# Optimization experiments

Measured on AMD Instinct MI355X. Metric: run time of the kernel, lower is better.

## Reference

```python
import jax, jax.numpy as jnp
import numpy as np

H = 4096          # hidden_size
NIN = 17          # RFSIZE*RFSIZE + ADDINPUT + NBACTIONS = 9+4+4
NA = 4            # NBACTIONS


def setup_inputs() -> dict:
    key = jax.random.key(0)
    ks = jax.random.split(key, 12)
    return {
        "x": jax.random.normal(ks[0], (1, NIN), jnp.float32),
        "hidden": 0.1 * jax.random.normal(ks[1], (1, H), jnp.float32),
        "hebb": 0.01 * jax.random.normal(ks[2], (H, H), jnp.float32),
        "i2h_w": 0.1 * jax.random.normal(ks[3], (H, NIN), jnp.float32),
        "i2h_b": 0.1 * jax.random.normal(ks[4], (H,), jnp.float32),
        "w": 0.01 * jax.random.uniform(ks[5], (H, H), jnp.float32),
        "alpha": 0.01 * jax.random.uniform(ks[6], (H, H), jnp.float32),
        "eta": 0.01 * jnp.ones((1,), jnp.float32),
        "h2o_w": 0.1 * jax.random.normal(ks[7], (NA, H), jnp.float32),
        "h2o_b": 0.1 * jax.random.normal(ks[8], (NA,), jnp.float32),
        "h2v_w": 0.1 * jax.random.normal(ks[9], (1, H), jnp.float32),
        "h2v_b": 0.1 * jax.random.normal(ks[10], (1,), jnp.float32),
    }


def reference(x, hidden, hebb, i2h_w, i2h_b, w, alpha, eta, h2o_w, h2o_b, h2v_w, h2v_b):
    # plastic RNN step: h = tanh(i2h(x) + hidden @ (w + alpha*hebb))
    h = jnp.tanh(x @ i2h_w.T + i2h_b + hidden @ (w + alpha * hebb))  # [1,H]
    # Hebbian trace update: (1-eta)*hebb + eta * outer(hidden, h)
    hebb_new = (1.0 - eta) * hebb + eta * (hidden[0][:, None] * h[0][None, :])  # [H,H]
    activout = jax.nn.softmax(h @ h2o_w.T + h2o_b, axis=-1)  # [1,NA]
    valueout = h @ h2v_w.T + h2v_b                           # [1,1]
    return activout, valueout, h, hebb_new
```

## Files before the change

### kernel.cpp

```cpp
#include <hip/hip_runtime.h>

#define HDIM 4096
#define NIN 17
#define NA 4

constexpr int TB = 256;
constexpr int CPT = 4;
constexpr int BXC = HDIM / (TB * CPT);
constexpr int NCHUNK = 256;
constexpr int RPC = HDIM / NCHUNK;
constexpr size_t NELEM = (size_t)HDIM * HDIM;

__global__ __launch_bounds__(TB, 4)
void k_matvec(const float* __restrict__ w, const float* __restrict__ alpha,
              const float* __restrict__ hebb, const float* __restrict__ hidden,
              float* __restrict__ partial, float* __restrict__ acc5) {
    if (blockIdx.x == 0 && blockIdx.y == 0 && threadIdx.x < 8) acc5[threadIdx.x] = 0.f;

    const int col0 = (blockIdx.x * TB + threadIdx.x) * CPT;
    const int row0 = blockIdx.y * RPC;
    const size_t base = (size_t)row0 * HDIM + col0;
    const float* __restrict__ wp = w + base;
    const float* __restrict__ ap = alpha + base;
    const float* __restrict__ bp = hebb + base;
    float4 acc = make_float4(0.f, 0.f, 0.f, 0.f);
#pragma unroll 8
    for (int r = 0; r < RPC; ++r) {
        const float hv = hidden[row0 + r];
        const size_t off = (size_t)r * HDIM;
        const float4 wv = *(const float4*)(wp + off);
        const float4 av = *(const float4*)(ap + off);
        const float4 bv = *(const float4*)(bp + off);
        acc.x += hv * (wv.x + av.x * bv.x);
        acc.y += hv * (wv.y + av.y * bv.y);
        acc.z += hv * (wv.z + av.z * bv.z);
        acc.w += hv * (wv.w + av.w * bv.w);
    }
    *(float4*)(partial + (size_t)blockIdx.y * HDIM + col0) = acc;
}

__global__ __launch_bounds__(256)
void k_hact(const float* __restrict__ partial, const float* __restrict__ x,
            const float* __restrict__ i2h_w, const float* __restrict__ i2h_b,
            const float* __restrict__ h2o_w, const float* __restrict__ h2v_w,
            float* __restrict__ h_f, float* __restrict__ h_out,
            float* __restrict__ acc5) {
    const int tid = threadIdx.x;
    const int j = blockIdx.x * 256 + tid;
    float s = 0.f;
#pragma unroll 16
    for (int c = 0; c < NCHUNK; ++c) s += partial[(size_t)c * HDIM + j];
    float z = i2h_b[j] + s;
#pragma unroll
    for (int k = 0; k < NIN; ++k) z += x[k] * i2h_w[j * NIN + k];
    const float h = tanhf(z);
    h_f[j] = h;
    h_out[j] = h;

    float d[NA + 1];
#pragma unroll
    for (int a = 0; a < NA; ++a) d[a] = h * h2o_w[(size_t)a * HDIM + j];
    d[NA] = h * h2v_w[j];

    __shared__ float red[256];
#pragma unroll
    for (int a = 0; a < NA + 1; ++a) {
        red[tid] = d[a];
        __syncthreads();
        for (int sft = 128; sft > 0; sft >>= 1) {
            if (tid < sft) red[tid] += red[tid + sft];
            __syncthreads();
        }
        if (tid == 0) atomicAdd(acc5 + a, red[0]);
        __syncthreads();
    }
}

__global__ __launch_bounds__(256)
void k_hebb(const float* __restrict__ hebb, const float* __restrict__ hidden,
            const float* __restrict__ h_f, const float* __restrict__ eta,
            float* __restrict__ hebb_out) {
    const size_t t = (size_t)blockIdx.x * 256 + threadIdx.x;
    const size_t s = 4 * t + 3;
    const float e = eta[0];
    const float om = 1.f - e;

    if (t == 0) {
        const float hv0 = e * hidden[0];
        hebb_out[0] = om * hebb[0] + hv0 * h_f[0];
        hebb_out[1] = om * hebb[1] + hv0 * h_f[1];
        hebb_out[2] = om * hebb[2] + hv0 * h_f[2];
    }

    if (s + 3 < NELEM) {
        const float b0 = hebb[s];
        const float4 bv = *(const float4*)(hebb + s + 1);
        const float b[4] = {b0, bv.x, bv.y, bv.z};
        float v[4];
#pragma unroll
        for (int k = 0; k < 4; ++k) {
            const size_t m = s + (size_t)k;
            const int i = (int)(m >> 12);
            const int jj = (int)(m & (HDIM - 1));
            v[k] = om * b[k] + e * hidden[i] * h_f[jj];
        }
        *(float4*)(hebb_out + s) = make_float4(v[0], v[1], v[2], v[3]);
    } else {
        for (size_t m = s; m < NELEM; ++m) {
            const int i = (int)(m >> 12);
            const int jj = (int)(m & (HDIM - 1));
            hebb_out[m] = om * hebb[m] + e * hidden[i] * h_f[jj];
        }
    }
}

__global__ __launch_bounds__(64)
void k_finish(const float* __restrict__ acc5,
              const float* __restrict__ h2o_b, const float* __restrict__ h2v_b,
              float* __restrict__ out) {
    if (threadIdx.x == 0) {
        float o[NA];
        float mx = -1e30f;
#pragma unroll
        for (int a = 0; a < NA; ++a) { o[a] = acc5[a] + h2o_b[a]; mx = fmaxf(mx, o[a]); }
        float se = 0.f;
#pragma unroll
        for (int a = 0; a < NA; ++a) { o[a] = __expf(o[a] - mx); se += o[a]; }
#pragma unroll
        for (int a = 0; a < NA; ++a) out[a] = o[a] / se;
        out[NA] = acc5[NA] + h2v_b[0];
    }
}

extern "C" void kernel_launch(void* const* d_in, const int* in_sizes, int n_in,
                              void* d_out, int out_size, void* d_ws, size_t ws_size,
                              hipStream_t stream) {
    const float* x      = (const float*)d_in[0];
    const float* hidden = (const float*)d_in[1];
    const float* hebb   = (const float*)d_in[2];
    const float* i2h_w  = (const float*)d_in[3];
    const float* i2h_b  = (const float*)d_in[4];
    const float* w      = (const float*)d_in[5];
    const float* alpha  = (const float*)d_in[6];
    const float* eta    = (const float*)d_in[7];
    const float* h2o_w  = (const float*)d_in[8];
    const float* h2o_b  = (const float*)d_in[9];
    const float* h2v_w  = (const float*)d_in[10];
    const float* h2v_b  = (const float*)d_in[11];
    float* out = (float*)d_out;

    float* partial = (float*)d_ws;
    float* h_f  = partial + (size_t)NCHUNK * HDIM;
    float* acc5 = h_f + HDIM;

    float* h_out    = out + 5;
    float* hebb_out = out + 5 + HDIM;

    k_matvec<<<dim3(BXC, NCHUNK), TB, 0, stream>>>(w, alpha, hebb, hidden, partial, acc5);
    k_hact<<<HDIM / 256, 256, 0, stream>>>(partial, x, i2h_w, i2h_b, h2o_w, h2v_w, h_f, h_out, acc5);
    k_hebb<<<(int)((NELEM / 4) / 256), 256, 0, stream>>>(hebb, hidden, h_f, eta, hebb_out);
    k_finish<<<1, 64, 0, stream>>>(acc5, h2o_b, h2v_b, out);
}
```

Before: 272.3 us.

## Fuse whole plastic RNN step into one cooperative kernel keeping hebb in registers

Replaces the four-kernel pipeline with a single cooperative-launch kernel that uses grid-wide syncs between phases: the matvec partials, the column reduction with tanh, the output head, and the Hebbian update. Each thread keeps its 16 rows of hebb tiles in registers. The update phase reuses them instead of re-reading hebb from HBM, which cuts one full 64MB pass of memory traffic and removes the launch gaps. In exchange the kernel has higher register pressure, two grid-wide barriers, and scalar stores for the misaligned hebb output. It also relies on all 1024 blocks being co-resident; if the occupancy check fails, it falls back to the old path.

```diff
diff --git a/kernel.cpp b/kernel.cpp
--- a/kernel.cpp
+++ b/kernel.cpp
@@ -1,4 +1,7 @@
 #include <hip/hip_runtime.h>
+#include <hip/hip_cooperative_groups.h>
+
+namespace cg = cooperative_groups;
 
 #define HDIM 4096
 #define NIN 17
@@ -12,17 +15,140 @@
 constexpr size_t NELEM = (size_t)HDIM * HDIM;
 
 __global__ __launch_bounds__(TB, 4)
+void k_fused(const float* __restrict__ w, const float* __restrict__ alpha,
+             const float* __restrict__ hebb, const float* __restrict__ hidden,
+             const float* __restrict__ x, const float* __restrict__ i2h_w,
+             const float* __restrict__ i2h_b,
+             const float* __restrict__ h2o_w, const float* __restrict__ h2o_b,
+             const float* __restrict__ h2v_w, const float* __restrict__ h2v_b,
+             const float* __restrict__ eta,
+             float* __restrict__ partial, float* __restrict__ h_f,
+             float* __restrict__ out) {
+    const int tid = threadIdx.x;
+    const int bx = blockIdx.x;
+    const int by = blockIdx.y;
+    const int col0 = (bx * TB + tid) * CPT;
+    const int row0 = by * RPC;
+
+    __shared__ float4 red4[TB];
+    __shared__ float redh[TB];
+
+    const size_t base = (size_t)row0 * HDIM + col0;
+    const float* wp = w + base;
+    const float* ap = alpha + base;
+    const float* bp = hebb + base;
+
+    float4 hb[RPC];
+#pragma unroll
+    for (int r = 0; r < RPC; ++r)
+        hb[r] = *(const float4*)(bp + (size_t)r * HDIM);
+
+    float4 wv[2], av[2];
+    wv[0] = *(const float4*)(wp);
+    av[0] = *(const float4*)(ap);
+    float4 acc = make_float4(0.f, 0.f, 0.f, 0.f);
+#pragma unroll
+    for (int r = 0; r < RPC; ++r) {
+        if (r + 1 < RPC) {
+            wv[(r + 1) & 1] = *(const float4*)(wp + (size_t)(r + 1) * HDIM);
+            av[(r + 1) & 1] = *(const float4*)(ap + (size_t)(r + 1) * HDIM);
+        }
+        const float hv = hidden[row0 + r];
+        const float4 wv0 = wv[r & 1], av0 = av[r & 1], bv0 = hb[r];
+        acc.x += hv * (wv0.x + av0.x * bv0.x);
+        acc.y += hv * (wv0.y + av0.y * bv0.y);
+        acc.z += hv * (wv0.z + av0.z * bv0.z);
+        acc.w += hv * (wv0.w + av0.w * bv0.w);
+    }
+    *(float4*)(partial + (size_t)by * HDIM + col0) = acc;
+
+    cg::this_grid().sync();
+
+    const int flat = by * BXC + bx;
+    const int j0 = flat * 4;
+    red4[tid] = *(const float4*)(partial + (size_t)tid * HDIM + j0);
+    __syncthreads();
+    for (int s = 128; s > 0; s >>= 1) {
+        if (tid < s) {
+            float4 m = red4[tid], o = red4[tid + s];
+            m.x += o.x; m.y += o.y; m.z += o.z; m.w += o.w;
+            red4[tid] = m;
+        }
+        __syncthreads();
+    }
+    if (tid < 4) {
+        const int j = j0 + tid;
+        float z = ((const float*)red4)[tid] + i2h_b[j];
+#pragma unroll
+        for (int k = 0; k < NIN; ++k) z += x[k] * i2h_w[j * NIN + k];
+        const float h = tanhf(z);
+        h_f[j] = h;
+        out[5 + j] = h;
+    }
+
+    cg::this_grid().sync();
+
+    if (flat == BXC * NCHUNK - 1) {
+        float a5[NA + 1] = {0.f, 0.f, 0.f, 0.f, 0.f};
+        for (int t = tid; t < HDIM; t += TB) {
+            const float hv = h_f[t];
+#pragma unroll
+            for (int a = 0; a < NA; ++a) a5[a] += hv * h2o_w[(size_t)a * HDIM + t];
+            a5[NA] += hv * h2v_w[t];
+        }
+        float res[NA + 1];
+#pragma unroll
+        for (int a = 0; a <= NA; ++a) {
+            redh[tid] = a5[a];
+            __syncthreads();
+            for (int s = 128; s > 0; s >>= 1) {
+                if (tid < s) redh[tid] += redh[tid + s];
+                __syncthreads();
+            }
+            if (tid == 0) res[a] = redh[0];
+            __syncthreads();
+        }
+        if (tid == 0) {
+            float o[NA];
+            float mx = -1e30f;
+#pragma unroll
+            for (int a = 0; a < NA; ++a) { o[a] = res[a] + h2o_b[a]; mx = fmaxf(mx, o[a]); }
+            float se = 0.f;
+#pragma unroll
+            for (int a = 0; a < NA; ++a) { o[a] = __expf(o[a] - mx); se += o[a]; }
+#pragma unroll
+            for (int a = 0; a < NA; ++a) out[a] = o[a] / se;
+            out[NA] = res[NA] + h2v_b[0];
+        }
+    }
+
+    const float e = eta[0];
+    const float om = 1.f - e;
+    const float4 hvv = *(const float4*)(h_f + col0);
+    float* hebb_out = out + 5 + HDIM;
+#pragma unroll
+    for (int r = 0; r < RPC; ++r) {
+        const float hi = e * hidden[row0 + r];
+        const size_t m = (size_t)(row0 + r) * HDIM + col0;
+        const float4 b = hb[r];
+        hebb_out[m]     = om * b.x + hi * hvv.x;
+        hebb_out[m + 1] = om * b.y + hi * hvv.y;
+        hebb_out[m + 2] = om * b.z + hi * hvv.z;
+        hebb_out[m + 3] = om * b.w + hi * hvv.w;
+    }
+}
+
+__global__ __launch_bounds__(TB, 4)
 void k_matvec(const float* __restrict__ w, const float* __restrict__ alpha,
               const float* __restrict__ hebb, const float* __restrict__ hidden,
               float* __restrict__ partial, float* __restrict__ acc5) {
     if (blockIdx.x == 0 && blockIdx.y == 0 && threadIdx.x < 8) acc5[threadIdx.x] = 0.f;
-
     const int col0 = (blockIdx.x * TB + threadIdx.x) * CPT;
     const int row0 = blockIdx.y * RPC;
     const size_t base = (size_t)row0 * HDIM + col0;
-    const float* __restrict__ wp = w + base;
-    const float* __restrict__ ap = alpha + base;
-    const float* __restrict__ bp = hebb + base;
+    const float* wp = w + base;
+    const float* ap = alpha + base;
+    const float* bp = hebb + base;
     float4 acc = make_float4(0.f, 0.f, 0.f, 0.f);
 #pragma unroll 8
     for (int r = 0; r < RPC; ++r) {
@@ -56,12 +182,10 @@
     const float h = tanhf(z);
     h_f[j] = h;
     h_out[j] = h;
-
     float d[NA + 1];
 #pragma unroll
     for (int a = 0; a < NA; ++a) d[a] = h * h2o_w[(size_t)a * HDIM + j];
     d[NA] = h * h2v_w[j];
-
     __shared__ float red[256];
 #pragma unroll
     for (int a = 0; a < NA + 1; ++a) {
@@ -84,14 +208,12 @@
     const size_t s = 4 * t + 3;
     const float e = eta[0];
     const float om = 1.f - e;
-
     if (t == 0) {
         const float hv0 = e * hidden[0];
         hebb_out[0] = om * hebb[0] + hv0 * h_f[0];
         hebb_out[1] = om * hebb[1] + hv0 * h_f[1];
         hebb_out[2] = om * hebb[2] + hv0 * h_f[2];
     }
-
     if (s + 3 < NELEM) {
         const float b0 = hebb[s];
         const float4 bv = *(const float4*)(hebb + s + 1);
@@ -156,8 +278,23 @@
     float* h_out    = out + 5;
     float* hebb_out = out + 5 + HDIM;
 
-    k_matvec<<<dim3(BXC, NCHUNK), TB, 0, stream>>>(w, alpha, hebb, hidden, partial, acc5);
-    k_hact<<<HDIM / 256, 256, 0, stream>>>(partial, x, i2h_w, i2h_b, h2o_w, h2v_w, h_f, h_out, acc5);
-    k_hebb<<<(int)((NELEM / 4) / 256), 256, 0, stream>>>(hebb, hidden, h_f, eta, hebb_out);
-    k_finish<<<1, 64, 0, stream>>>(acc5, h2o_b, h2v_b, out);
-}
+    static int coop = -1;
+    if (coop < 0) {
+        int maxb = 0;
+        hipError_t err = hipOccupancyMaxActiveBlocksPerMultiprocessor(&maxb, k_fused, TB, 0);
+        coop = (err == hipSuccess && maxb >= 4) ? 1 : 0;
+    }
+
+    if (coop) {
+        void* args[] = {(void*)&w, (void*)&alpha, (void*)&hebb, (void*)&hidden,
+                        (void*)&x, (void*)&i2h_w, (void*)&i2h_b,
+                        (void*)&h2o_w, (void*)&h2o_b, (void*)&h2v_w, (void*)&h2v_b,
+                        (void*)&eta, (void*)&partial, (void*)&h_f, (void*)&out};
+        hipLaunchCooperativeKernel(k_fused, dim3(BXC, NCHUNK), dim3(TB), args, 0, stream);
+    } else {
+        k_matvec<<<dim3(BXC, NCHUNK), TB, 0, stream>>>(w, alpha, hebb, hidden, partial, acc5);
+        k_hact<<<HDIM / 256, 256, 0, stream>>>(partial, x, i2h_w, i2h_b, h2o_w, h2v_w, h_f, h_out, acc5);
+        k_hebb<<<(int)((NELEM / 4) / 256), 256, 0, stream>>>(hebb, hidden, h_f, eta, hebb_out);
+        k_finish<<<1, 64, 0, stream>>>(acc5, h2o_b, h2v_b, out);
+    }
+}
```

New measurement: 273.6 us. About the same (+0.5%).

## Restructure matvec loads, split-K reduction, and use nontemporal memory ops

Applied to the files above, without the earlier changes.

The matvec kernel now splits rows into 1024 chunks of 4 rows each. Each thread issues all of its w, alpha and hebb loads before computing, and the w and alpha loads are nontemporal. The activation kernel spreads the partial-sum reduction across 8 groups per 32 columns, using shared memory and then wave shuffles instead of one serial loop per column. The hebb update uses nontemporal stores, and the partial buffer now lives in the not-yet-written hebb output region. The finer split quadruples the partial-sum traffic in exchange for more parallelism and memory-level parallelism.

```diff
diff --git a/kernel.cpp b/kernel.cpp
--- a/kernel.cpp
+++ b/kernel.cpp
@@ -4,83 +4,91 @@
 #define NIN 17
 #define NA 4
 
+using f4 = __attribute__((ext_vector_type(4))) float;
+
 constexpr int TB = 256;
 constexpr int CPT = 4;
 constexpr int BXC = HDIM / (TB * CPT);
-constexpr int NCHUNK = 256;
+constexpr int NCHUNK = 1024;
 constexpr int RPC = HDIM / NCHUNK;
 constexpr size_t NELEM = (size_t)HDIM * HDIM;
 
-__global__ __launch_bounds__(TB, 4)
-void k_matvec(const float* __restrict__ w, const float* __restrict__ alpha,
-              const float* __restrict__ hebb, const float* __restrict__ hidden,
-              float* __restrict__ partial, float* __restrict__ acc5) {
+__global__ void k_matvec(const float* __restrict__ w, const float* __restrict__ alpha,
+                         const float* __restrict__ hebb, const float* __restrict__ hidden,
+                         float* __restrict__ partial, float* __restrict__ acc5) {
     if (blockIdx.x == 0 && blockIdx.y == 0 && threadIdx.x < 8) acc5[threadIdx.x] = 0.f;
-
     const int col0 = (blockIdx.x * TB + threadIdx.x) * CPT;
     const int row0 = blockIdx.y * RPC;
     const size_t base = (size_t)row0 * HDIM + col0;
-    const float* __restrict__ wp = w + base;
-    const float* __restrict__ ap = alpha + base;
-    const float* __restrict__ bp = hebb + base;
-    float4 acc = make_float4(0.f, 0.f, 0.f, 0.f);
-#pragma unroll 8
+
+    f4 wv[RPC], av[RPC], bv[RPC];
+#pragma unroll
+    for (int r = 0; r < RPC; ++r) {
+        const size_t off = base + (size_t)r * HDIM;
+        wv[r] = __builtin_nontemporal_load((const f4*)(w + off));
+        av[r] = __builtin_nontemporal_load((const f4*)(alpha + off));
+        bv[r] = *(const f4*)(hebb + off);
+    }
+    f4 acc = {0.f, 0.f, 0.f, 0.f};
+#pragma unroll
     for (int r = 0; r < RPC; ++r) {
         const float hv = hidden[row0 + r];
-        const size_t off = (size_t)r * HDIM;
-        const float4 wv = *(const float4*)(wp + off);
-        const float4 av = *(const float4*)(ap + off);
-        const float4 bv = *(const float4*)(bp + off);
-        acc.x += hv * (wv.x + av.x * bv.x);
-        acc.y += hv * (wv.y + av.y * bv.y);
-        acc.z += hv * (wv.z + av.z * bv.z);
-        acc.w += hv * (wv.w + av.w * bv.w);
+        acc += hv * (wv[r] + av[r] * bv[r]);
     }
-    *(float4*)(partial + (size_t)blockIdx.y * HDIM + col0) = acc;
+    *(f4*)(partial + (size_t)blockIdx.y * HDIM + col0) = acc;
 }
 
-__global__ __launch_bounds__(256)
-void k_hact(const float* __restrict__ partial, const float* __restrict__ x,
-            const float* __restrict__ i2h_w, const float* __restrict__ i2h_b,
-            const float* __restrict__ h2o_w, const float* __restrict__ h2v_w,
-            float* __restrict__ h_f, float* __restrict__ h_out,
-            float* __restrict__ acc5) {
+constexpr int HC = 32;
+constexpr int HGRP = TB / HC;
+constexpr int HCPG = NCHUNK / HGRP;
+
+__global__ void k_hact(const float* __restrict__ partial, const float* __restrict__ x,
+                       const float* __restrict__ i2h_w, const float* __restrict__ i2h_b,
+                       const float* __restrict__ h2o_w, const float* __restrict__ h2v_w,
+                       float* __restrict__ h_f, float* __restrict__ h_out,
+                       float* __restrict__ acc5) {
     const int tid = threadIdx.x;
-    const int j = blockIdx.x * 256 + tid;
+    const int lane = tid & (HC - 1);
+    const int grp = tid >> 5;
+    const int col = blockIdx.x * HC + lane;
+
     float s = 0.f;
+    const float* p = partial + (size_t)(grp * HCPG) * HDIM + col;
 #pragma unroll 16
-    for (int c = 0; c < NCHUNK; ++c) s += partial[(size_t)c * HDIM + j];
-    float z = i2h_b[j] + s;
+    for (int c = 0; c < HCPG; ++c) s += p[(size_t)c * HDIM];
+
+    __shared__ float red[TB];
+    red[tid] = s;
+    __syncthreads();
+    for (int st = TB / 2; st >= HC; st >>= 1) {
+        if (tid < st) red[tid] += red[tid + st];
+        __syncthreads();
+    }
+    if (tid < HC) {
+        float z = red[tid] + i2h_b[col];
 #pragma unroll
-    for (int k = 0; k < NIN; ++k) z += x[k] * i2h_w[j * NIN + k];
-    const float h = tanhf(z);
-    h_f[j] = h;
-    h_out[j] = h;
-
-    float d[NA + 1];
+        for (int k = 0; k < NIN; ++k) z += x[k] * i2h_w[col * NIN + k];
+        const float h = tanhf(z);
+        h_f[col] = h;
+        h_out[col] = h;
+        float d[NA + 1];
 #pragma unroll
-    for (int a = 0; a < NA; ++a) d[a] = h * h2o_w[(size_t)a * HDIM + j];
-    d[NA] = h * h2v_w[j];
-
-    __shared__ float red[256];
+        for (int a = 0; a < NA; ++a) d[a] = h * h2o_w[(size_t)a * HDIM + col];
+        d[NA] = h * h2v_w[col];
 #pragma unroll
-    for (int a = 0; a < NA + 1; ++a) {
-        red[tid] = d[a];
-        __syncthreads();
-        for (int sft = 128; sft > 0; sft >>= 1) {
-            if (tid < sft) red[tid] += red[tid + sft];
-            __syncthreads();
+        for (int a = 0; a <= NA; ++a) {
+            float v = d[a];
+#pragma unroll
+            for (int sft = 16; sft > 0; sft >>= 1) v += __shfl_down(v, sft, 32);
+            if (lane == 0) atomicAdd(acc5 + a, v);
         }
-        if (tid == 0) atomicAdd(acc5 + a, red[0]);
-        __syncthreads();
     }
 }
 
-__global__ __launch_bounds__(256)
-void k_hebb(const float* __restrict__ hebb, const float* __restrict__ hidden,
-            const float* __restrict__ h_f, const float* __restrict__ eta,
-            float* __restrict__ hebb_out) {
-    const size_t t = (size_t)blockIdx.x * 256 + threadIdx.x;
+__global__ void k_hebb(const float* __restrict__ hebb, const float* __restrict__ hidden,
+                       const float* __restrict__ h_f, const float* __restrict__ eta,
+                       float* __restrict__ hebb_out) {
+    const size_t t = (size_t)blockIdx.x * TB + threadIdx.x;
     const size_t s = 4 * t + 3;
     const float e = eta[0];
     const float om = 1.f - e;
@@ -94,9 +102,9 @@
 
     if (s + 3 < NELEM) {
         const float b0 = hebb[s];
-        const float4 bv = *(const float4*)(hebb + s + 1);
+        const f4 bv = *(const f4*)(hebb + s + 1);
         const float b[4] = {b0, bv.x, bv.y, bv.z};
-        float v[4];
+        f4 v;
 #pragma unroll
         for (int k = 0; k < 4; ++k) {
             const size_t m = s + (size_t)k;
@@ -104,7 +112,7 @@
             const int jj = (int)(m & (HDIM - 1));
             v[k] = om * b[k] + e * hidden[i] * h_f[jj];
         }
-        *(float4*)(hebb_out + s) = make_float4(v[0], v[1], v[2], v[3]);
+        __builtin_nontemporal_store(v, (f4*)(hebb_out + s));
     } else {
         for (size_t m = s; m < NELEM; ++m) {
             const int i = (int)(m >> 12);
@@ -149,15 +157,16 @@
     const float* h2v_b  = (const float*)d_in[11];
     float* out = (float*)d_out;
 
-    float* partial = (float*)d_ws;
-    float* h_f  = partial + (size_t)NCHUNK * HDIM;
-    float* acc5 = h_f + HDIM;
-
     float* h_out    = out + 5;
     float* hebb_out = out + 5 + HDIM;
 
+    float* partial = out + 8192;
+
+    float* h_f  = (float*)d_ws;
+    float* acc5 = h_f + HDIM;
+
     k_matvec<<<dim3(BXC, NCHUNK), TB, 0, stream>>>(w, alpha, hebb, hidden, partial, acc5);
-    k_hact<<<HDIM / 256, 256, 0, stream>>>(partial, x, i2h_w, i2h_b, h2o_w, h2v_w, h_f, h_out, acc5);
-    k_hebb<<<(int)((NELEM / 4) / 256), 256, 0, stream>>>(hebb, hidden, h_f, eta, hebb_out);
+    k_hact<<<HDIM / HC, TB, 0, stream>>>(partial, x, i2h_w, i2h_b, h2o_w, h2v_w, h_f, h_out, acc5);
+    k_hebb<<<(int)((NELEM / 4) / TB), TB, 0, stream>>>(hebb, hidden, h_f, eta, hebb_out);
     k_finish<<<1, 64, 0, stream>>>(acc5, h2o_b, h2v_b, out);
 }
```

After: 255.7 us. 6.1% less time.
